# Optimization experiments

Hardware: AMD Instinct MI355X
Metric: run time of the kernel (lower is better)

Reference implementation:

```python
import jax, jax.numpy as jnp
import numpy as np

D_MODEL = 512
N_HEADS = 8
EDGE_FEAT_DIM = 4
NUM_GRAPHS = 64
NODES_PER_GRAPH = 128
N_NODES = NUM_GRAPHS * NODES_PER_GRAPH          # 8192
EDGES_PER_GRAPH = 4096                           # avg degree 32
N_EDGES = NUM_GRAPHS * EDGES_PER_GRAPH           # 262144


def setup_inputs() -> dict:
    key = jax.random.key(0)
    ks = jax.random.split(key, 12)
    s = 0.02
    x = jax.random.normal(ks[0], (N_NODES, D_MODEL), jnp.float32)
    # edges constrained within their graph (block-diagonal structure)
    g_of_e = jnp.arange(N_EDGES, dtype=jnp.int32) // EDGES_PER_GRAPH
    src = g_of_e * NODES_PER_GRAPH + jax.random.randint(ks[1], (N_EDGES,), 0, NODES_PER_GRAPH, jnp.int32)
    dst = g_of_e * NODES_PER_GRAPH + jax.random.randint(ks[2], (N_EDGES,), 0, NODES_PER_GRAPH, jnp.int32)
    edge_index = jnp.stack([src, dst]).astype(jnp.int32)
    edge_attr = jax.random.normal(ks[3], (N_EDGES, EDGE_FEAT_DIM), jnp.float32)
    batch = jnp.repeat(jnp.arange(NUM_GRAPHS, dtype=jnp.int32), NODES_PER_GRAPH)
    # projection weights (in,out) convention: y = x @ W + b
    Wq = jax.random.normal(ks[4], (D_MODEL, D_MODEL), jnp.float32) * s
    Wk = jax.random.normal(ks[5], (D_MODEL, D_MODEL), jnp.float32) * s
    Wv = jax.random.normal(ks[6], (D_MODEL, D_MODEL), jnp.float32) * s
    Wo = jax.random.normal(ks[7], (D_MODEL, D_MODEL), jnp.float32) * s
    bq = jnp.zeros((D_MODEL,), jnp.float32)
    bk = jnp.zeros((D_MODEL,), jnp.float32)
    bv = jnp.zeros((D_MODEL,), jnp.float32)
    bo = jnp.zeros((D_MODEL,), jnp.float32)
    # edge bias MLP: edge_feat_dim -> d_model -> n_heads
    W1 = jax.random.normal(ks[8], (EDGE_FEAT_DIM, D_MODEL), jnp.float32) * s
    b1 = jnp.zeros((D_MODEL,), jnp.float32)
    W2 = jax.random.normal(ks[9], (D_MODEL, N_HEADS), jnp.float32) * s
    b2 = jnp.zeros((N_HEADS,), jnp.float32)
    return {"x": x, "edge_index": edge_index, "edge_attr": edge_attr, "batch": batch,
            "n_g": NODES_PER_GRAPH,
            "Wq": Wq, "bq": bq, "Wk": Wk, "bk": bk, "Wv": Wv, "bv": bv,
            "Wo": Wo, "bo": bo, "W1": W1, "b1": b1, "W2": W2, "b2": b2}


def reference(x, edge_index, edge_attr, batch, n_g, Wq, bq, Wk, bk, Wv, bv, Wo, bo, W1, b1, W2, b2):
    # batch is contiguous equal-size blocks of n_g nodes per graph, so the
    # per-graph Python loop of the original collapses to a batched (G, n_g)
    # block-diagonal attention. Dropout is identity (eval / p used only in train).
    N, d_model = x.shape
    H = W2.shape[1]
    d_k = d_model // H
    G = N // n_g
    scale = 1.0 / float(np.sqrt(d_k))

    Q = (x @ Wq + bq).reshape(G, n_g, H, d_k)
    K = (x @ Wk + bk).reshape(G, n_g, H, d_k)
    V = (x @ Wv + bv).reshape(G, n_g, H, d_k)

    # (G, i, j, h) dense per-graph scores
    scores = jnp.einsum('gihd,gjhd->gijh', Q, K) * scale

    # edge bias: MLP(edge_attr) -> (E, H), scattered at (graph, local_src, local_dst)
    bias = jax.nn.relu(edge_attr @ W1 + b1) @ W2 + b2
    ge = edge_index[0] // n_g
    ls = edge_index[0] % n_g
    ld = edge_index[1] % n_g
    scores = scores.at[ge, ls, ld].add(bias)

    attn = jax.nn.softmax(scores, axis=2)  # softmax over j (keys), matches dim=1 of (i,j,h)
    out = jnp.einsum('gijh,gjhd->gihd', attn, V).reshape(N, d_model)
    return out @ Wo + bo
```

## Files before the change

### kernel.cpp

```cpp
#include <hip/hip_runtime.h>
#include <hip/hip_bf16.h>

#define E_TOTAL 262144
#define NG      128
#define GRAPHS  64
#define NHEADS  8
#define DKH     64
#define DMODEL  512
#define NNODES  8192

typedef __bf16 bf16x8 __attribute__((ext_vector_type(8)));
typedef float  f32x4  __attribute__((ext_vector_type(4)));
typedef short  s16x4  __attribute__((ext_vector_type(4)));
typedef unsigned short u16x8 __attribute__((ext_vector_type(8)));

typedef __attribute__((address_space(3))) char lds_char;
typedef const __attribute__((address_space(1))) char glb_char;

__device__ inline __hip_bfloat16 f2hbf(float f) { return __float2bfloat16(f); }
__device__ inline unsigned short f2u16(float f) {
    return __builtin_bit_cast(unsigned short, __float2bfloat16(f));
}
__device__ inline __bf16 f2bf(float f) {
    return __builtin_bit_cast(__bf16, f2u16(f));
}
__device__ inline bf16x8 cvt8(float4 lo, float4 hi) {
    bf16x8 o;
    o[0] = f2bf(lo.x); o[1] = f2bf(lo.y); o[2] = f2bf(lo.z); o[3] = f2bf(lo.w);
    o[4] = f2bf(hi.x); o[5] = f2bf(hi.y); o[6] = f2bf(hi.z); o[7] = f2bf(hi.w);
    return o;
}

__global__ __launch_bounds__(256) void prep_kernel(
    const float* __restrict__ Wq, const float* __restrict__ Wk,
    const float* __restrict__ Wv, const float* __restrict__ Wo,
    const float* __restrict__ W1, const float* __restrict__ b1,
    const float* __restrict__ W2, const float* __restrict__ b2,
    const float* __restrict__ x, __hip_bfloat16* __restrict__ xbf,
    __hip_bfloat16* __restrict__ wqkvt, __hip_bfloat16* __restrict__ wot,
    __hip_bfloat16* __restrict__ w1fragt, float* __restrict__ b1f,
    __hip_bfloat16* __restrict__ w2at, float* __restrict__ b2f)
{
    int blk = blockIdx.x, tid = threadIdx.x;
    if (blk < 256) {
        __shared__ __align__(16) __hip_bfloat16 tile[64][65];
        const float* src;
        __hip_bfloat16* dstT;
        int n0, k0, nb;
        if (blk < 192) {
            int nt = blk % 24, ktile = blk / 24;
            n0 = nt * 64; k0 = ktile * 64;
            if (n0 < 512)       { src = Wq; nb = n0; }
            else if (n0 < 1024) { src = Wk; nb = n0 - 512; }
            else                { src = Wv; nb = n0 - 1024; }
            dstT = wqkvt;
        } else {
            int t = blk - 192;
            n0 = (t % 8) * 64; k0 = (t / 8) * 64; nb = n0;
            src = Wo; dstT = wot;
        }
        #pragma unroll
        for (int i = 0; i < 16; ++i) {
            int idx = tid + i * 256;
            int kr = idx >> 6, nc = idx & 63;
            tile[kr][nc] = f2hbf(src[(size_t)(k0 + kr) * 512 + nb + nc]);
        }
        __syncthreads();
        #pragma unroll
        for (int i = 0; i < 16; ++i) {
            int idx = tid + i * 256;
            int nr = idx >> 6, kc = idx & 63;
            dstT[(size_t)(n0 + nr) * 512 + k0 + kc] = tile[kc][nr];
        }
    } else if (blk == 256) {
        __hip_bfloat16 z = f2hbf(0.f);
        for (int n = tid; n < 512; n += 256) {
            #pragma unroll
            for (int j = 0; j < 4; ++j) w1fragt[n * 4 + j] = f2hbf(W1[(size_t)j * 512 + n]);
        }
        for (int i = tid; i < 512; i += 256) b1f[i] = b1[i];
        for (int i = tid; i < 32 * 64 * 4; i += 256) {
            int t = i >> 8, lane = (i >> 2) & 63, j = i & 3;
            int q = lane >> 4, l = lane & 15;
            w2at[i] = (l < 8) ? f2hbf(W2[(size_t)(16 * t + 4 * q + j) * 8 + l]) : z;
        }
        if (tid < 8) b2f[tid] = b2[tid];
    } else {
        int base = (blk - 257) * 2048 + tid * 8;
        float4 lo = *(const float4*)(x + base);
        float4 hi = *(const float4*)(x + base + 4);
        *(bf16x8*)(xbf + base) = cvt8(lo, hi);
    }
}

__device__ __forceinline__ void gemm0_body(
    const __hip_bfloat16* __restrict__ A, const __hip_bfloat16* __restrict__ BT,
    int row0, int col0,
    const float* __restrict__ bq, const float* __restrict__ bk,
    const float* __restrict__ bv,
    __hip_bfloat16* __restrict__ qkv, __hip_bfloat16* __restrict__ vt,
    __hip_bfloat16* __restrict__ As, __hip_bfloat16* __restrict__ Bs)
{
    const int K = 512;
    int tid = threadIdx.x;
    int lane = tid & 63, quad = lane >> 4, l16 = lane & 15;
    int wave = tid >> 6, wi = wave >> 1, wj = wave & 1;

    f32x4 acc[4][4];
    #pragma unroll
    for (int a = 0; a < 4; a++)
        #pragma unroll
        for (int b = 0; b < 4; b++)
            #pragma unroll
            for (int r = 0; r < 4; r++) acc[a][b][r] = 0.f;

    const __hip_bfloat16* Ag0 = A + (size_t)(row0 + (tid >> 2)) * K + (tid & 3) * 8;
    const __hip_bfloat16* Ag1 = Ag0 + (size_t)64 * K;
    const __hip_bfloat16* Bg0 = BT + (size_t)(col0 + (tid >> 2)) * K + (tid & 3) * 8;
    const __hip_bfloat16* Bg1 = Bg0 + (size_t)64 * K;
    char* AsB = (char*)As;
    char* BsB = (char*)Bs;

    __builtin_amdgcn_global_load_lds((glb_char*)Ag0, (lds_char*)(AsB + tid * 16), 16, 0, 0);
    __builtin_amdgcn_global_load_lds((glb_char*)Ag1, (lds_char*)(AsB + 4096 + tid * 16), 16, 0, 0);
    __builtin_amdgcn_global_load_lds((glb_char*)Bg0, (lds_char*)(BsB + tid * 16), 16, 0, 0);
    __builtin_amdgcn_global_load_lds((glb_char*)Bg1, (lds_char*)(BsB + 4096 + tid * 16), 16, 0, 0);
    __syncthreads();

    #pragma unroll 2
    for (int kt = 0; kt < 16; ++kt) {
        int cur = kt & 1, nxt = cur ^ 1;
        if (kt < 15) {
            __builtin_amdgcn_global_load_lds((glb_char*)(Ag0 + (kt + 1) * 32),
                (lds_char*)(AsB + nxt * 8192 + tid * 16), 16, 0, 0);
            __builtin_amdgcn_global_load_lds((glb_char*)(Ag1 + (kt + 1) * 32),
                (lds_char*)(AsB + nxt * 8192 + 4096 + tid * 16), 16, 0, 0);
            __builtin_amdgcn_global_load_lds((glb_char*)(Bg0 + (kt + 1) * 32),
                (lds_char*)(BsB + nxt * 8192 + tid * 16), 16, 0, 0);
            __builtin_amdgcn_global_load_lds((glb_char*)(Bg1 + (kt + 1) * 32),
                (lds_char*)(BsB + nxt * 8192 + 4096 + tid * 16), 16, 0, 0);
        }
        const __hip_bfloat16* Asc = As + cur * 4096;
        const __hip_bfloat16* Bsc = Bs + cur * 4096;
        bf16x8 af[4], bfr[4];
        #pragma unroll
        for (int t = 0; t < 4; t++)
            af[t] = *(const bf16x8*)&Asc[(wi * 64 + t * 16 + l16) * 32 + quad * 8];
        #pragma unroll
        for (int t = 0; t < 4; t++)
            bfr[t] = *(const bf16x8*)&Bsc[(wj * 64 + t * 16 + l16) * 32 + quad * 8];
        #pragma unroll
        for (int ti = 0; ti < 4; ti++)
            #pragma unroll
            for (int tj = 0; tj < 4; tj++)
                acc[ti][tj] = __builtin_amdgcn_mfma_f32_16x16x32_bf16(af[ti], bfr[tj], acc[ti][tj], 0, 0, 0);
        __syncthreads();
    }

    #pragma unroll
    for (int ti = 0; ti < 4; ti++)
        #pragma unroll
        for (int tj = 0; tj < 4; tj++) {
            int c = col0 + wj * 64 + tj * 16 + l16;
            #pragma unroll
            for (int r = 0; r < 4; r++) {
                int rw = row0 + wi * 64 + ti * 16 + quad * 4 + r;
                float v = acc[ti][tj][r];
                if (c < 1024) {
                    v += (c < 512) ? bq[c] : bk[c - 512];
                    qkv[(size_t)rw * 1536 + c] = f2hbf(v);
                } else {
                    v += bv[c - 1024];
                    int g = rw >> 7, i = rw & 127, hh = (c - 1024) >> 6, d = (c - 1024) & 63;
                    vt[(((size_t)(g * 8 + hh)) * 64 + d) * 128 + i] = f2hbf(v);
                }
            }
        }
}

__device__ __forceinline__ void edge_body(
    int eblk,
    const float* __restrict__ ea,
    const __hip_bfloat16* __restrict__ w1fragt, const float* __restrict__ b1f,
    const __hip_bfloat16* __restrict__ w2at, const float* __restrict__ b2f,
    float* __restrict__ biasE)
{
    int tid = threadIdx.x, wave = tid >> 6, lane = tid & 63;
    int quad = lane >> 4, l16 = lane & 15;
    int eb = eblk * 256 + wave * 64;

    s16x4 eaf[4] = {};
    if (quad == 0) {
        #pragma unroll
        for (int gg = 0; gg < 4; ++gg) {
            float4 e4 = *(const float4*)(ea + (size_t)(eb + gg * 16 + l16) * 4);
            eaf[gg][0] = (short)f2u16(e4.x); eaf[gg][1] = (short)f2u16(e4.y);
            eaf[gg][2] = (short)f2u16(e4.z); eaf[gg][3] = (short)f2u16(e4.w);
        }
    }

    f32x4 c2[4];
    #pragma unroll
    for (int gg = 0; gg < 4; ++gg)
        #pragma unroll
        for (int r = 0; r < 4; ++r) c2[gg][r] = 0.f;

    #pragma unroll 4
    for (int t = 0; t < 32; ++t) {
        s16x4 a1 = *(const s16x4*)(w1fragt + ((size_t)t * 16 + l16) * 4);
        float4 b14 = *(const float4*)(b1f + t * 16 + quad * 4);
        s16x4 a2 = *(const s16x4*)(w2at + ((size_t)t * 64 + lane) * 4);
        #pragma unroll
        for (int gg = 0; gg < 4; ++gg) {
            f32x4 c1 = {0.f, 0.f, 0.f, 0.f};
            c1 = __builtin_amdgcn_mfma_f32_16x16x16bf16_1k(a1, eaf[gg], c1, 0, 0, 0);
            s16x4 hfrag;
            hfrag[0] = (short)f2u16(fmaxf(c1[0] + b14.x, 0.f));
            hfrag[1] = (short)f2u16(fmaxf(c1[1] + b14.y, 0.f));
            hfrag[2] = (short)f2u16(fmaxf(c1[2] + b14.z, 0.f));
            hfrag[3] = (short)f2u16(fmaxf(c1[3] + b14.w, 0.f));
            c2[gg] = __builtin_amdgcn_mfma_f32_16x16x16bf16_1k(a2, hfrag, c2[gg], 0, 0, 0);
        }
    }
    if (quad < 2) {
        #pragma unroll
        for (int gg = 0; gg < 4; ++gg) {
            #pragma unroll
            for (int r = 0; r < 4; ++r) {
                int hh = quad * 4 + r;
                biasE[(size_t)hh * E_TOTAL + eb + gg * 16 + l16] = c2[gg][r] + b2f[hh];
            }
        }
    }
}

__global__ __launch_bounds__(256) void mega_kernel(
    const __hip_bfloat16* __restrict__ A, const __hip_bfloat16* __restrict__ BT,
    const float* __restrict__ bq, const float* __restrict__ bk,
    const float* __restrict__ bv,
    __hip_bfloat16* __restrict__ qkv, __hip_bfloat16* __restrict__ vt,
    const float* __restrict__ ea,
    const __hip_bfloat16* __restrict__ w1fragt, const float* __restrict__ b1f,
    const __hip_bfloat16* __restrict__ w2at, const float* __restrict__ b2f,
    float* __restrict__ biasE)
{
    __shared__ __align__(16) __hip_bfloat16 As[2 * 128 * 32];
    __shared__ __align__(16) __hip_bfloat16 Bs[2 * 128 * 32];
    int blk = blockIdx.x;
    if (blk < 768) {
        gemm0_body(A, BT, (blk & 63) * 128, (blk >> 6) * 128,
                   bq, bk, bv, qkv, vt, As, Bs);
    } else {
        edge_body(blk - 768, ea, w1fragt, b1f, w2at, b2f, biasE);
    }
}

__global__ __launch_bounds__(256) void gemm1_kernel(
    const __hip_bfloat16* __restrict__ A, const __hip_bfloat16* __restrict__ BT,
    const float* __restrict__ bo, float* __restrict__ out)
{
    const int K = 512;
    __shared__ __align__(16) __hip_bfloat16 As[2 * 128 * 32];
    __shared__ __align__(16) __hip_bfloat16 Bs[2 * 64 * 32];
    int tid = threadIdx.x;
    int lane = tid & 63, quad = lane >> 4, l16 = lane & 15;
    int wave = tid >> 6, wi = wave >> 1, wj = wave & 1;
    int row0 = blockIdx.x * 128, col0 = blockIdx.y * 64;

    f32x4 acc[4][2];
    #pragma unroll
    for (int a = 0; a < 4; a++)
        #pragma unroll
        for (int b = 0; b < 2; b++)
            #pragma unroll
            for (int r = 0; r < 4; r++) acc[a][b][r] = 0.f;

    const __hip_bfloat16* Ag0 = A + (size_t)(row0 + (tid >> 2)) * K + (tid & 3) * 8;
    const __hip_bfloat16* Ag1 = Ag0 + (size_t)64 * K;
    const __hip_bfloat16* Bg  = BT + (size_t)(col0 + (tid >> 2)) * K + (tid & 3) * 8;
    char* AsB = (char*)As;
    char* BsB = (char*)Bs;

    __builtin_amdgcn_global_load_lds((glb_char*)Ag0, (lds_char*)(AsB + tid * 16), 16, 0, 0);
    __builtin_amdgcn_global_load_lds((glb_char*)Ag1, (lds_char*)(AsB + 4096 + tid * 16), 16, 0, 0);
    __builtin_amdgcn_global_load_lds((glb_char*)Bg,  (lds_char*)(BsB + tid * 16), 16, 0, 0);
    __syncthreads();

    #pragma unroll 2
    for (int kt = 0; kt < 16; ++kt) {
        int cur = kt & 1, nxt = cur ^ 1;
        if (kt < 15) {
            __builtin_amdgcn_global_load_lds((glb_char*)(Ag0 + (kt + 1) * 32),
                (lds_char*)(AsB + nxt * 8192 + tid * 16), 16, 0, 0);
            __builtin_amdgcn_global_load_lds((glb_char*)(Ag1 + (kt + 1) * 32),
                (lds_char*)(AsB + nxt * 8192 + 4096 + tid * 16), 16, 0, 0);
            __builtin_amdgcn_global_load_lds((glb_char*)(Bg + (kt + 1) * 32),
                (lds_char*)(BsB + nxt * 4096 + tid * 16), 16, 0, 0);
        }
        const __hip_bfloat16* Asc = As + cur * 4096;
        const __hip_bfloat16* Bsc = Bs + cur * 2048;
        bf16x8 af[4], bfr[2];
        #pragma unroll
        for (int t = 0; t < 4; t++)
            af[t] = *(const bf16x8*)&Asc[(wi * 64 + t * 16 + l16) * 32 + quad * 8];
        #pragma unroll
        for (int t = 0; t < 2; t++)
            bfr[t] = *(const bf16x8*)&Bsc[(wj * 32 + t * 16 + l16) * 32 + quad * 8];
        #pragma unroll
        for (int ti = 0; ti < 4; ti++)
            #pragma unroll
            for (int tj = 0; tj < 2; tj++)
                acc[ti][tj] = __builtin_amdgcn_mfma_f32_16x16x32_bf16(af[ti], bfr[tj], acc[ti][tj], 0, 0, 0);
        __syncthreads();
    }

    #pragma unroll
    for (int ti = 0; ti < 4; ti++)
        #pragma unroll
        for (int tj = 0; tj < 2; tj++) {
            int c = col0 + wj * 32 + tj * 16 + l16;
            #pragma unroll
            for (int r = 0; r < 4; r++) {
                int rw = row0 + wi * 64 + ti * 16 + quad * 4 + r;
                out[(size_t)rw * 512 + c] = acc[ti][tj][r] + bo[c];
            }
        }
}

#define SS 132
__global__ __launch_bounds__(256) void attn_kernel(
    const __hip_bfloat16* __restrict__ qkv,
    const __hip_bfloat16* __restrict__ vt,
    const float* __restrict__ biasE,
    const int* __restrict__ eidx,
    __hip_bfloat16* __restrict__ O)
{
    __shared__ __align__(16) float S[128 * SS];
    int blk = blockIdx.x, g = blk & 63, h = blk >> 6;
    int tid = threadIdx.x, wave = tid >> 6, lane = tid & 63;
    int quad = lane >> 4, l16 = lane & 15;

    int   sa[16];
    float bv[16];
    #pragma unroll
    for (int u = 0; u < 16; ++u) {
        int idx = g * 4096 + tid + u * 256;
        int ls = eidx[idx] & 127;
        int ld = eidx[E_TOTAL + idx] & 127;
        sa[u] = ls * SS + ld;
        bv[u] = biasE[(size_t)h * E_TOTAL + idx];
    }

    const __hip_bfloat16* qbase = qkv + (size_t)(g * 128) * 1536 + h * 64;
    const __hip_bfloat16* kbase = qbase + 512;

    f32x4 acc[2][8];
    #pragma unroll
    for (int t = 0; t < 2; t++)
        #pragma unroll
        for (int j = 0; j < 8; j++)
            #pragma unroll
            for (int r = 0; r < 4; r++) acc[t][j][r] = 0.f;

    #pragma unroll
    for (int k0 = 0; k0 < 64; k0 += 32) {
        bf16x8 af[2];
        #pragma unroll
        for (int t = 0; t < 2; t++) {
            int m = wave * 32 + t * 16 + l16;
            af[t] = *(const bf16x8*)(qbase + (size_t)m * 1536 + k0 + quad * 8);
        }
        #pragma unroll
        for (int tj = 0; tj < 8; tj++) {
            int n = tj * 16 + l16;
            bf16x8 bfr = *(const bf16x8*)(kbase + (size_t)n * 1536 + k0 + quad * 8);
            #pragma unroll
            for (int t = 0; t < 2; t++)
                acc[t][tj] = __builtin_amdgcn_mfma_f32_16x16x32_bf16(af[t], bfr, acc[t][tj], 0, 0, 0);
        }
    }
    #pragma unroll
    for (int t = 0; t < 2; t++)
        #pragma unroll
        for (int tj = 0; tj < 8; tj++)
            #pragma unroll
            for (int r = 0; r < 4; r++) {
                int i = wave * 32 + t * 16 + quad * 4 + r;
                int j = tj * 16 + l16;
                S[i * SS + j] = acc[t][tj][r] * 0.125f;
            }
    __syncthreads();

    #pragma unroll
    for (int u = 0; u < 16; ++u)
        atomicAdd(&S[sa[u]], bv[u]);
    __syncthreads();

    #pragma unroll 4
    for (int r = wave * 32; r < wave * 32 + 32; ++r) {
        float2 v = *(const float2*)&S[r * SS + 2 * lane];
        float m = fmaxf(v.x, v.y);
        #pragma unroll
        for (int off = 32; off > 0; off >>= 1) m = fmaxf(m, __shfl_xor(m, off));
        float e0 = __expf(v.x - m), e1 = __expf(v.y - m);
        float s = e0 + e1;
        #pragma unroll
        for (int off = 32; off > 0; off >>= 1) s += __shfl_xor(s, off);
        float inv = 1.0f / s;
        float2 o; o.x = e0 * inv; o.y = e1 * inv;
        *(float2*)&S[r * SS + 2 * lane] = o;
    }
    __syncthreads();

    f32x4 oacc[2][4];
    #pragma unroll
    for (int t = 0; t < 2; t++)
        #pragma unroll
        for (int j = 0; j < 4; j++)
            #pragma unroll
            for (int r = 0; r < 4; r++) oacc[t][j][r] = 0.f;

    const __hip_bfloat16* vbase = vt + (size_t)(g * 8 + h) * 64 * 128;
    #pragma unroll
    for (int k0 = 0; k0 < 128; k0 += 32) {
        bf16x8 af[2];
        #pragma unroll
        for (int t = 0; t < 2; t++) {
            int m = wave * 32 + t * 16 + l16;
            const float* p = &S[m * SS + k0 + quad * 8];
            f32x4 xa = *(const f32x4*)p;
            f32x4 xb = *(const f32x4*)(p + 4);
            bf16x8 a;
            a[0] = f2bf(xa[0]); a[1] = f2bf(xa[1]); a[2] = f2bf(xa[2]); a[3] = f2bf(xa[3]);
            a[4] = f2bf(xb[0]); a[5] = f2bf(xb[1]); a[6] = f2bf(xb[2]); a[7] = f2bf(xb[3]);
            af[t] = a;
        }
        #pragma unroll
        for (int tj = 0; tj < 4; tj++) {
            int d = tj * 16 + l16;
            bf16x8 bfr = *(const bf16x8*)(vbase + (size_t)d * 128 + k0 + quad * 8);
            #pragma unroll
            for (int t = 0; t < 2; t++)
                oacc[t][tj] = __builtin_amdgcn_mfma_f32_16x16x32_bf16(af[t], bfr, oacc[t][tj], 0, 0, 0);
        }
    }
    #pragma unroll
    for (int t = 0; t < 2; t++)
        #pragma unroll
        for (int tj = 0; tj < 4; tj++)
            #pragma unroll
            for (int r = 0; r < 4; r++) {
                int i = wave * 32 + t * 16 + quad * 4 + r;
                int d = tj * 16 + l16;
                O[(size_t)(g * 128 + i) * 512 + h * 64 + d] = f2hbf(oacc[t][tj][r]);
            }
}

#define WS_WQKVT 0x0
#define WS_WOT   0x180000
#define WS_W1FR  0x200000
#define WS_B1F   0x202000
#define WS_W2AT  0x202800
#define WS_B2F   0x206800
#define WS_QKV   0xA10000
#define WS_VT    0x2210000
#define WS_BIASE 0x2A10000
#define WS_O     0x3210000
#define WS_XBF   WS_O

extern "C" void kernel_launch(void* const* d_in, const int* in_sizes, int n_in,
                              void* d_out, int out_size, void* d_ws, size_t ws_size,
                              hipStream_t stream) {
    const float* x    = (const float*)d_in[0];
    const int*   eidx = (const int*)d_in[1];
    const float* ea   = (const float*)d_in[2];
    const float* Wq = (const float*)d_in[5];
    const float* bq = (const float*)d_in[6];
    const float* Wk = (const float*)d_in[7];
    const float* bk = (const float*)d_in[8];
    const float* Wv = (const float*)d_in[9];
    const float* bv = (const float*)d_in[10];
    const float* Wo = (const float*)d_in[11];
    const float* bo = (const float*)d_in[12];
    const float* W1 = (const float*)d_in[13];
    const float* b1 = (const float*)d_in[14];
    const float* W2 = (const float*)d_in[15];
    const float* b2 = (const float*)d_in[16];

    char* ws = (char*)d_ws;
    __hip_bfloat16* wqkvt   = (__hip_bfloat16*)(ws + WS_WQKVT);
    __hip_bfloat16* wot     = (__hip_bfloat16*)(ws + WS_WOT);
    __hip_bfloat16* w1fragt = (__hip_bfloat16*)(ws + WS_W1FR);
    float* b1f   = (float*)(ws + WS_B1F);
    __hip_bfloat16* w2at    = (__hip_bfloat16*)(ws + WS_W2AT);
    float* b2f   = (float*)(ws + WS_B2F);
    __hip_bfloat16* qkv = (__hip_bfloat16*)(ws + WS_QKV);
    __hip_bfloat16* vt  = (__hip_bfloat16*)(ws + WS_VT);
    float* biasE = (float*)(ws + WS_BIASE);
    __hip_bfloat16* O   = (__hip_bfloat16*)(ws + WS_O);
    __hip_bfloat16* xbf = (__hip_bfloat16*)(ws + WS_XBF);

    prep_kernel<<<257 + 2048, 256, 0, stream>>>(Wq, Wk, Wv, Wo, W1, b1, W2, b2,
                                                x, xbf,
                                                wqkvt, wot, w1fragt, b1f, w2at, b2f);
    mega_kernel<<<768 + E_TOTAL / 256, 256, 0, stream>>>(
        xbf, wqkvt, bq, bk, bv, qkv, vt,
        ea, w1fragt, b1f, w2at, b2f, biasE);
    attn_kernel<<<GRAPHS * NHEADS, 256, 0, stream>>>(qkv, vt, biasE, eidx, O);
    gemm1_kernel<<<dim3(NNODES / 128, 512 / 64), 256, 0, stream>>>(
        O, wot, bo, (float*)d_out);
}
```

Baseline: 217.3 us.

## Triple-buffer GEMM K-loop with vmcnt waits and widen attention blocks to 512 threads

Both GEMM kernels move from double-buffered global-to-LDS loads with two syncthreads per step to a three-stage ring. Each step waits on a partial vmcnt and uses a single barrier, so more loads stay in flight behind the MFMAs. The attention kernel now runs with 512 threads, 8 waves of 16 rows each instead of 4 waves of 32, which halves per-thread register and edge-scatter work and raises parallelism per block. In exchange, LDS use in the GEMMs grows by half, which may reduce occupancy. The hand-written vmcnt counts must match the number of loads issued per stage.

```diff
diff --git a/kernel.cpp b/kernel.cpp
--- a/kernel.cpp
+++ b/kernel.cpp
@@ -121,27 +121,24 @@
     char* AsB = (char*)As;
     char* BsB = (char*)Bs;
 
-    __builtin_amdgcn_global_load_lds((glb_char*)Ag0, (lds_char*)(AsB + tid * 16), 16, 0, 0);
-    __builtin_amdgcn_global_load_lds((glb_char*)Ag1, (lds_char*)(AsB + 4096 + tid * 16), 16, 0, 0);
-    __builtin_amdgcn_global_load_lds((glb_char*)Bg0, (lds_char*)(BsB + tid * 16), 16, 0, 0);
-    __builtin_amdgcn_global_load_lds((glb_char*)Bg1, (lds_char*)(BsB + 4096 + tid * 16), 16, 0, 0);
-    __syncthreads();
-
-    #pragma unroll 2
+#define G0STAGE(kt, buf) do { \
+    __builtin_amdgcn_global_load_lds((glb_char*)(Ag0 + (kt) * 32), (lds_char*)(AsB + (buf) * 8192 + tid * 16), 16, 0, 0); \
+    __builtin_amdgcn_global_load_lds((glb_char*)(Ag1 + (kt) * 32), (lds_char*)(AsB + (buf) * 8192 + 4096 + tid * 16), 16, 0, 0); \
+    __builtin_amdgcn_global_load_lds((glb_char*)(Bg0 + (kt) * 32), (lds_char*)(BsB + (buf) * 8192 + tid * 16), 16, 0, 0); \
+    __builtin_amdgcn_global_load_lds((glb_char*)(Bg1 + (kt) * 32), (lds_char*)(BsB + (buf) * 8192 + 4096 + tid * 16), 16, 0, 0); \
+} while (0)
+
+    G0STAGE(0, 0);
+    G0STAGE(1, 1);
+
+    #pragma unroll
     for (int kt = 0; kt < 16; ++kt) {
-        int cur = kt & 1, nxt = cur ^ 1;
-        if (kt < 15) {
-            __builtin_amdgcn_global_load_lds((glb_char*)(Ag0 + (kt + 1) * 32),
-                (lds_char*)(AsB + nxt * 8192 + tid * 16), 16, 0, 0);
-            __builtin_amdgcn_global_load_lds((glb_char*)(Ag1 + (kt + 1) * 32),
-                (lds_char*)(AsB + nxt * 8192 + 4096 + tid * 16), 16, 0, 0);
-            __builtin_amdgcn_global_load_lds((glb_char*)(Bg0 + (kt + 1) * 32),
-                (lds_char*)(BsB + nxt * 8192 + tid * 16), 16, 0, 0);
-            __builtin_amdgcn_global_load_lds((glb_char*)(Bg1 + (kt + 1) * 32),
-                (lds_char*)(BsB + nxt * 8192 + 4096 + tid * 16), 16, 0, 0);
-        }
-        const __hip_bfloat16* Asc = As + cur * 4096;
-        const __hip_bfloat16* Bsc = Bs + cur * 4096;
+        if (kt < 15) asm volatile("s_waitcnt vmcnt(4)" ::: "memory");
+        else         asm volatile("s_waitcnt vmcnt(0)" ::: "memory");
+        __builtin_amdgcn_s_barrier();
+        if (kt < 14) G0STAGE(kt + 2, (kt + 2) % 3);
+        const __hip_bfloat16* Asc = As + (kt % 3) * 4096;
+        const __hip_bfloat16* Bsc = Bs + (kt % 3) * 4096;
         bf16x8 af[4], bfr[4];
         #pragma unroll
         for (int t = 0; t < 4; t++)
@@ -154,8 +151,8 @@
             #pragma unroll
             for (int tj = 0; tj < 4; tj++)
                 acc[ti][tj] = __builtin_amdgcn_mfma_f32_16x16x32_bf16(af[ti], bfr[tj], acc[ti][tj], 0, 0, 0);
-        __syncthreads();
-    }
+    }
+#undef G0STAGE
 
     #pragma unroll
     for (int ti = 0; ti < 4; ti++)
@@ -244,8 +241,8 @@
     const __hip_bfloat16* __restrict__ w2at, const float* __restrict__ b2f,
     float* __restrict__ biasE)
 {
-    __shared__ __align__(16) __hip_bfloat16 As[2 * 128 * 32];
-    __shared__ __align__(16) __hip_bfloat16 Bs[2 * 128 * 32];
+    __shared__ __align__(16) __hip_bfloat16 As[3 * 128 * 32];
+    __shared__ __align__(16) __hip_bfloat16 Bs[3 * 128 * 32];
     int blk = blockIdx.x;
     if (blk < 768) {
         gemm0_body(A, BT, (blk & 63) * 128, (blk >> 6) * 128,
@@ -260,8 +257,8 @@
     const float* __restrict__ bo, float* __restrict__ out)
 {
     const int K = 512;
-    __shared__ __align__(16) __hip_bfloat16 As[2 * 128 * 32];
-    __shared__ __align__(16) __hip_bfloat16 Bs[2 * 64 * 32];
+    __shared__ __align__(16) __hip_bfloat16 As[3 * 128 * 32];
+    __shared__ __align__(16) __hip_bfloat16 Bs[3 * 64 * 32];
     int tid = threadIdx.x;
     int lane = tid & 63, quad = lane >> 4, l16 = lane & 15;
     int wave = tid >> 6, wi = wave >> 1, wj = wave & 1;
@@ -281,24 +278,23 @@
     char* AsB = (char*)As;
     char* BsB = (char*)Bs;
 
-    __builtin_amdgcn_global_load_lds((glb_char*)Ag0, (lds_char*)(AsB + tid * 16), 16, 0, 0);
-    __builtin_amdgcn_global_load_lds((glb_char*)Ag1, (lds_char*)(AsB + 4096 + tid * 16), 16, 0, 0);
-    __builtin_amdgcn_global_load_lds((glb_char*)Bg,  (lds_char*)(BsB + tid * 16), 16, 0, 0);
-    __syncthreads();
-
-    #pragma unroll 2
+#define G1STAGE(kt, buf) do { \
+    __builtin_amdgcn_global_load_lds((glb_char*)(Ag0 + (kt) * 32), (lds_char*)(AsB + (buf) * 8192 + tid * 16), 16, 0, 0); \
+    __builtin_amdgcn_global_load_lds((glb_char*)(Ag1 + (kt) * 32), (lds_char*)(AsB + (buf) * 8192 + 4096 + tid * 16), 16, 0, 0); \
+    __builtin_amdgcn_global_load_lds((glb_char*)(Bg + (kt) * 32),  (lds_char*)(BsB + (buf) * 4096 + tid * 16), 16, 0, 0); \
+} while (0)
+
+    G1STAGE(0, 0);
+    G1STAGE(1, 1);
+
+    #pragma unroll
     for (int kt = 0; kt < 16; ++kt) {
-        int cur = kt & 1, nxt = cur ^ 1;
-        if (kt < 15) {
-            __builtin_amdgcn_global_load_lds((glb_char*)(Ag0 + (kt + 1) * 32),
-                (lds_char*)(AsB + nxt * 8192 + tid * 16), 16, 0, 0);
-            __builtin_amdgcn_global_load_lds((glb_char*)(Ag1 + (kt + 1) * 32),
-                (lds_char*)(AsB + nxt * 8192 + 4096 + tid * 16), 16, 0, 0);
-            __builtin_amdgcn_global_load_lds((glb_char*)(Bg + (kt + 1) * 32),
-                (lds_char*)(BsB + nxt * 4096 + tid * 16), 16, 0, 0);
-        }
-        const __hip_bfloat16* Asc = As + cur * 4096;
-        const __hip_bfloat16* Bsc = Bs + cur * 2048;
+        if (kt < 15) asm volatile("s_waitcnt vmcnt(3)" ::: "memory");
+        else         asm volatile("s_waitcnt vmcnt(0)" ::: "memory");
+        __builtin_amdgcn_s_barrier();
+        if (kt < 14) G1STAGE(kt + 2, (kt + 2) % 3);
+        const __hip_bfloat16* Asc = As + (kt % 3) * 4096;
+        const __hip_bfloat16* Bsc = Bs + (kt % 3) * 2048;
         bf16x8 af[4], bfr[2];
         #pragma unroll
         for (int t = 0; t < 4; t++)
@@ -311,8 +307,8 @@
             #pragma unroll
             for (int tj = 0; tj < 2; tj++)
                 acc[ti][tj] = __builtin_amdgcn_mfma_f32_16x16x32_bf16(af[ti], bfr[tj], acc[ti][tj], 0, 0, 0);
-        __syncthreads();
-    }
+    }
+#undef G1STAGE
 
     #pragma unroll
     for (int ti = 0; ti < 4; ti++)
@@ -328,7 +324,7 @@
 }
 
 #define SS 132
-__global__ __launch_bounds__(256) void attn_kernel(
+__global__ __launch_bounds__(512) void attn_kernel(
     const __hip_bfloat16* __restrict__ qkv,
     const __hip_bfloat16* __restrict__ vt,
     const float* __restrict__ biasE,
@@ -340,64 +336,54 @@
     int tid = threadIdx.x, wave = tid >> 6, lane = tid & 63;
     int quad = lane >> 4, l16 = lane & 15;
 
-    int   sa[16];
-    float bv[16];
-    #pragma unroll
-    for (int u = 0; u < 16; ++u) {
-        int idx = g * 4096 + tid + u * 256;
+    int   sa[8];
+    float bvv[8];
+    #pragma unroll
+    for (int u = 0; u < 8; ++u) {
+        int idx = g * 4096 + tid + u * 512;
         int ls = eidx[idx] & 127;
         int ld = eidx[E_TOTAL + idx] & 127;
         sa[u] = ls * SS + ld;
-        bv[u] = biasE[(size_t)h * E_TOTAL + idx];
+        bvv[u] = biasE[(size_t)h * E_TOTAL + idx];
     }
 
     const __hip_bfloat16* qbase = qkv + (size_t)(g * 128) * 1536 + h * 64;
     const __hip_bfloat16* kbase = qbase + 512;
 
-    f32x4 acc[2][8];
-    #pragma unroll
-    for (int t = 0; t < 2; t++)
-        #pragma unroll
-        for (int j = 0; j < 8; j++)
-            #pragma unroll
-            for (int r = 0; r < 4; r++) acc[t][j][r] = 0.f;
+    f32x4 acc[8];
+    #pragma unroll
+    for (int j = 0; j < 8; j++)
+        #pragma unroll
+        for (int r = 0; r < 4; r++) acc[j][r] = 0.f;
 
     #pragma unroll
     for (int k0 = 0; k0 < 64; k0 += 32) {
-        bf16x8 af[2];
-        #pragma unroll
-        for (int t = 0; t < 2; t++) {
-            int m = wave * 32 + t * 16 + l16;
-            af[t] = *(const bf16x8*)(qbase + (size_t)m * 1536 + k0 + quad * 8);
-        }
+        int m = wave * 16 + l16;
+        bf16x8 af = *(const bf16x8*)(qbase + (size_t)m * 1536 + k0 + quad * 8);
         #pragma unroll
         for (int tj = 0; tj < 8; tj++) {
             int n = tj * 16 + l16;
             bf16x8 bfr = *(const bf16x8*)(kbase + (size_t)n * 1536 + k0 + quad * 8);
-            #pragma unroll
-            for (int t = 0; t < 2; t++)
-                acc[t][tj] = __builtin_amdgcn_mfma_f32_16x16x32_bf16(af[t], bfr, acc[t][tj], 0, 0, 0);
-        }
-    }
-    #pragma unroll
-    for (int t = 0; t < 2; t++)
-        #pragma unroll
-        for (int tj = 0; tj < 8; tj++)
-            #pragma unroll
-            for (int r = 0; r < 4; r++) {
-                int i = wave * 32 + t * 16 + quad * 4 + r;
-                int j = tj * 16 + l16;
-                S[i * SS + j] = acc[t][tj][r] * 0.125f;
-            }
+            acc[tj] = __builtin_amdgcn_mfma_f32_16x16x32_bf16(af, bfr, acc[tj], 0, 0, 0);
+        }
+    }
+    #pragma unroll
+    for (int tj = 0; tj < 8; tj++)
+        #pragma unroll
+        for (int r = 0; r < 4; r++) {
+            int i = wave * 16 + quad * 4 + r;
+            int j = tj * 16 + l16;
+            S[i * SS + j] = acc[tj][r] * 0.125f;
+        }
     __syncthreads();
 
     #pragma unroll
-    for (int u = 0; u < 16; ++u)
-        atomicAdd(&S[sa[u]], bv[u]);
+    for (int u = 0; u < 8; ++u)
+        atomicAdd(&S[sa[u]], bvv[u]);
     __syncthreads();
 
     #pragma unroll 4
-    for (int r = wave * 32; r < wave * 32 + 32; ++r) {
+    for (int r = wave * 16; r < wave * 16 + 16; ++r) {
         float2 v = *(const float2*)&S[r * SS + 2 * lane];
         float m = fmaxf(v.x, v.y);
         #pragma unroll
@@ -412,48 +398,37 @@
     }
     __syncthreads();
 
-    f32x4 oacc[2][4];
-    #pragma unroll
-    for (int t = 0; t < 2; t++)
-        #pragma unroll
-        for (int j = 0; j < 4; j++)
-            #pragma unroll
-            for (int r = 0; r < 4; r++) oacc[t][j][r] = 0.f;
+    f32x4 oacc[4];
+    #pragma unroll
+    for (int j = 0; j < 4; j++)
+        #pragma unroll
+        for (int r = 0; r < 4; r++) oacc[j][r] = 0.f;
 
     const __hip_bfloat16* vbase = vt + (size_t)(g * 8 + h) * 64 * 128;
     #pragma unroll
     for (int k0 = 0; k0 < 128; k0 += 32) {
-        bf16x8 af[2];
-        #pragma unroll
-        for (int t = 0; t < 2; t++) {
-            int m = wave * 32 + t * 16 + l16;
-            const float* p = &S[m * SS + k0 + quad * 8];
-            f32x4 xa = *(const f32x4*)p;
-            f32x4 xb = *(const f32x4*)(p + 4);
-            bf16x8 a;
-            a[0] = f2bf(xa[0]); a[1] = f2bf(xa[1]); a[2] = f2bf(xa[2]); a[3] = f2bf(xa[3]);
-            a[4] = f2bf(xb[0]); a[5] = f2bf(xb[1]); a[6] = f2bf(xb[2]); a[7] = f2bf(xb[3]);
-            af[t] = a;
-        }
+        int m = wave * 16 + l16;
+        const float* p = &S[m * SS + k0 + quad * 8];
+        f32x4 xa = *(const f32x4*)p;
+        f32x4 xb = *(const f32x4*)(p + 4);
+        bf16x8 af;
+        af[0] = f2bf(xa[0]); af[1] = f2bf(xa[1]); af[2] = f2bf(xa[2]); af[3] = f2bf(xa[3]);
+        af[4] = f2bf(xb[0]); af[5] = f2bf(xb[1]); af[6] = f2bf(xb[2]); af[7] = f2bf(xb[3]);
         #pragma unroll
         for (int tj = 0; tj < 4; tj++) {
             int d = tj * 16 + l16;
             bf16x8 bfr = *(const bf16x8*)(vbase + (size_t)d * 128 + k0 + quad * 8);
-            #pragma unroll
-            for (int t = 0; t < 2; t++)
-                oacc[t][tj] = __builtin_amdgcn_mfma_f32_16x16x32_bf16(af[t], bfr, oacc[t][tj], 0, 0, 0);
-        }
-    }
-    #pragma unroll
-    for (int t = 0; t < 2; t++)
-        #pragma unroll
-        for (int tj = 0; tj < 4; tj++)
-            #pragma unroll
-            for (int r = 0; r < 4; r++) {
-                int i = wave * 32 + t * 16 + quad * 4 + r;
-                int d = tj * 16 + l16;
-                O[(size_t)(g * 128 + i) * 512 + h * 64 + d] = f2hbf(oacc[t][tj][r]);
-            }
+            oacc[tj] = __builtin_amdgcn_mfma_f32_16x16x32_bf16(af, bfr, oacc[tj], 0, 0, 0);
+        }
+    }
+    #pragma unroll
+    for (int tj = 0; tj < 4; tj++)
+        #pragma unroll
+        for (int r = 0; r < 4; r++) {
+            int i = wave * 16 + quad * 4 + r;
+            int d = tj * 16 + l16;
+            O[(size_t)(g * 128 + i) * 512 + h * 64 + d] = f2hbf(oacc[tj][r]);
+        }
 }
 
 #define WS_WQKVT 0x0
@@ -506,7 +481,7 @@
     mega_kernel<<<768 + E_TOTAL / 256, 256, 0, stream>>>(
         xbf, wqkvt, bq, bk, bv, qkv, vt,
         ea, w1fragt, b1f, w2at, b2f, biasE);
-    attn_kernel<<<GRAPHS * NHEADS, 256, 0, stream>>>(qkv, vt, biasE, eidx, O);
+    attn_kernel<<<GRAPHS * NHEADS, 512, 0, stream>>>(qkv, vt, biasE, eidx, O);
     gemm1_kernel<<<dim3(NNODES / 128, 512 / 64), 256, 0, stream>>>(
         O, wot, bo, (float*)d_out);
 }
```

After: 211.6 us. -2.6%, faster.
